# Kernel optimization log

Measured on AMD Instinct MI355X. Metric: run time of the kernel, lower is better.

## Reference

```python
import jax, jax.numpy as jnp
import numpy as np

D_MODEL = 512
N_HEAD = 8
D_K = D_MODEL // N_HEAD
B, S = 4, 2048


def setup_inputs() -> dict:
    key = jax.random.key(0)
    ks = jax.random.split(key, 13)
    scale = 1.0 / np.sqrt(D_MODEL)
    inp = {
        "query": jax.random.normal(ks[0], (B, S, D_MODEL), jnp.float32),
        "key": jax.random.normal(ks[1], (B, S, D_MODEL), jnp.float32),
        "value": jax.random.normal(ks[2], (B, S, D_MODEL), jnp.float32),
        "mask": jax.random.randint(ks[3], (B, S, S), 0, 2).astype(bool),
        "Wq": jax.random.normal(ks[4], (D_MODEL, D_MODEL), jnp.float32) * scale,
        "bq": jax.random.normal(ks[5], (D_MODEL,), jnp.float32) * scale,
        "Wk": jax.random.normal(ks[6], (D_MODEL, D_MODEL), jnp.float32) * scale,
        "bk": jax.random.normal(ks[7], (D_MODEL,), jnp.float32) * scale,
        "Wv": jax.random.normal(ks[8], (D_MODEL, D_MODEL), jnp.float32) * scale,
        "bv": jax.random.normal(ks[9], (D_MODEL,), jnp.float32) * scale,
        "Wo": jax.random.normal(ks[10], (D_MODEL, D_MODEL), jnp.float32) * scale,
        "bo": jax.random.normal(ks[11], (D_MODEL,), jnp.float32) * scale,
    }
    return inp


def reference(query, key, value, mask, Wq, bq, Wk, bk, Wv, bv, Wo, bo):
    b = query.shape[0]
    # QKV projections -> [b, h, s, d_k]
    q = (query @ Wq.T + bq).reshape(b, -1, N_HEAD, D_K).transpose(0, 2, 1, 3)
    k = (key @ Wk.T + bk).reshape(b, -1, N_HEAD, D_K).transpose(0, 2, 1, 3)
    v = (value @ Wv.T + bv).reshape(b, -1, N_HEAD, D_K).transpose(0, 2, 1, 3)
    # scaled dot-product scores [b, h, sq, sk]
    scores = jnp.einsum("bhqd,bhkd->bhqk", q, k) / jnp.sqrt(jnp.float32(D_K))
    # masked_fill(mask, -1e4): mask broadcast over heads
    scores = jnp.where(mask[:, None, :, :], jnp.float32(-10000.0), scores)
    attn = jax.nn.softmax(scores, axis=-1)
    x = jnp.einsum("bhqk,bhkd->bhqd", attn, v)
    x = x.transpose(0, 2, 1, 3).reshape(b, -1, N_HEAD * D_K)
    return x @ Wo.T + bo
```

## Files before the change

kernel.cpp:

```cpp
#include <hip/hip_runtime.h>
#include <hip/hip_bf16.h>

#define DMODEL 512
#define NHEAD  8
#define DKH    64
#define SEQ    2048
#define NB     4
#define LOG2E  1.44269504088896f

typedef float f32x4 __attribute__((ext_vector_type(4)));
typedef float f32x16 __attribute__((ext_vector_type(16)));
typedef short bf16x8 __attribute__((ext_vector_type(8)));

__device__ __forceinline__ unsigned short f2bf(float x) {
    unsigned int u = __float_as_uint(x);
    u += 0x7fffu + ((u >> 16) & 1u);
    return (unsigned short)(u >> 16);
}

__device__ __forceinline__ void gload16(const void* g, void* l) {
    __builtin_amdgcn_global_load_lds(
        (const __attribute__((address_space(1))) unsigned int*)g,
        (__attribute__((address_space(3))) unsigned int*)l, 16, 0, 0);
}

__device__ __forceinline__ unsigned int cvtpk(float lo, float hi) {
    unsigned int r;
    asm("v_cvt_pk_bf16_f32 %0, %1, %2" : "=v"(r) : "v"(lo), "v"(hi));
    return r;
}

#define CVT_BLOCKS  512
#define PACK_BLOCKS 1024
struct PrepArgs {
    const float* src[4]; unsigned short* dst[4];
    const unsigned char* mask; unsigned long long* bits;
};

__global__ __launch_bounds__(256) void prep(PrepArgs a)
{
    const int bx = blockIdx.x;
    if (bx < CVT_BLOCKS) {
        const int seg = bx >> 7, base = bx & 127;
        const int i = (base * 256 + threadIdx.x) * 8;
        const float* s = a.src[seg];
        const float4 v0 = *reinterpret_cast<const float4*>(s + i);
        const float4 v1 = *reinterpret_cast<const float4*>(s + i + 4);
        ushort4 h0, h1;
        h0.x = f2bf(v0.x); h0.y = f2bf(v0.y); h0.z = f2bf(v0.z); h0.w = f2bf(v0.w);
        h1.x = f2bf(v1.x); h1.y = f2bf(v1.y); h1.z = f2bf(v1.z); h1.w = f2bf(v1.w);
        *reinterpret_cast<ushort4*>(a.dst[seg] + i)     = h0;
        *reinterpret_cast<ushort4*>(a.dst[seg] + i + 4) = h1;
    } else {
        __shared__ int anyb;
        if (threadIdx.x == 0) anyb = 0;
        __syncthreads();
        const uint4 dv = *reinterpret_cast<const uint4*>(a.mask + threadIdx.x * 16);
        if ((dv.x | dv.y | dv.z | dv.w) & 0xFFFFFF00u) atomicOr(&anyb, 1);
        __syncthreads();
        const int bytemode = anyb;

        const int w = (bx - CVT_BLOCKS) * 256 + threadIdx.x;
        const int b = w >> 16, kt = (w >> 11) & 31, row = w & 2047;
        const size_t eoff = ((size_t)(b * SEQ + row)) * SEQ + kt * 64;
        unsigned long long word = 0;
        if (bytemode) {
            const unsigned char* mp = a.mask + eoff;
            #pragma unroll
            for (int c = 0; c < 4; ++c) {
                const uint4 v = *reinterpret_cast<const uint4*>(mp + c * 16);
                const unsigned int n0 = (v.x | (v.x >> 7) | (v.x >> 14) | (v.x >> 21)) & 0xFu;
                const unsigned int n1 = (v.y | (v.y >> 7) | (v.y >> 14) | (v.y >> 21)) & 0xFu;
                const unsigned int n2 = (v.z | (v.z >> 7) | (v.z >> 14) | (v.z >> 21)) & 0xFu;
                const unsigned int n3 = (v.w | (v.w >> 7) | (v.w >> 14) | (v.w >> 21)) & 0xFu;
                const unsigned int ch = n0 | (n1 << 4) | (n2 << 8) | (n3 << 12);
                word |= (unsigned long long)ch << (16 * c);
            }
        } else {
            const unsigned int* mp = (const unsigned int*)a.mask + eoff;
            #pragma unroll
            for (int c = 0; c < 16; ++c) {
                const uint4 v = *reinterpret_cast<const uint4*>(mp + c * 4);
                const unsigned int nb = (v.x | (v.y << 1) | (v.z << 2) | (v.w << 3)) & 0xFu;
                word |= (unsigned long long)nb << (4 * c);
            }
        }
        a.bits[w] = word;
    }
}

struct GemmSet {
    const void* A; const unsigned short* W; const float* bias;
    unsigned short* outb; float* outf; float scale; int mode;
};
struct Gemm3 { GemmSet s[3]; };

template<int BM, bool AF32>
__global__ __launch_bounds__(256) void gemm_bf16(Gemm3 G)
{
    constexpr int NJ = (BM == 128) ? 4 : 2;
    __shared__ unsigned short As[BM * 64];
    __shared__ unsigned short Bs[128 * 64];

    const GemmSet gs = G.s[blockIdx.z];
    const int tid = threadIdx.x, lane = tid & 63, wv = tid >> 6;
    const int g = lane >> 4, lr = lane & 15;
    const int bm = blockIdx.x * BM, bn = blockIdx.y * 128;
    const int wm = (BM == 128) ? (wv & 1) * 64 : 0;
    const int wn = (BM == 128) ? (wv >> 1) * 64 : wv * 32;
    const int srow = lane >> 3;
    const int scol = 8 * ((lane & 7) ^ srow);

    const int arow  = tid >> 1;
    const int ahalf = tid & 1;

    f32x4 acc[4][NJ] = {};
    float4 ra[8];

    if constexpr (AF32) {
        const float* Af = (const float*)gs.A;
        #pragma unroll
        for (int j = 0; j < 4; ++j) {
            const size_t gb = (size_t)(bm + arow) * DMODEL + ahalf * 32 + j * 8;
            ra[2*j]   = *reinterpret_cast<const float4*>(&Af[gb]);
            ra[2*j+1] = *reinterpret_cast<const float4*>(&Af[gb + 4]);
        }
    }

    #pragma unroll
    for (int kt = 0; kt < DMODEL; kt += 64) {
        __syncthreads();
        if constexpr (AF32) {
            #pragma unroll
            for (int j = 0; j < 4; ++j) {
                unsigned int w0 = cvtpk(ra[2*j].x,   ra[2*j].y);
                unsigned int w1 = cvtpk(ra[2*j].z,   ra[2*j].w);
                unsigned int w2 = cvtpk(ra[2*j+1].x, ra[2*j+1].y);
                unsigned int w3 = cvtpk(ra[2*j+1].z, ra[2*j+1].w);
                uint4 pkd; pkd.x = w0; pkd.y = w1; pkd.z = w2; pkd.w = w3;
                const int boff = (arow * 128 + ahalf * 64 + j * 16) ^ ((arow & 7) << 4);
                *reinterpret_cast<uint4*>((char*)As + boff) = pkd;
            }
        } else {
            #pragma unroll
            for (int i = 0; i < BM / 32; ++i) {
                const int ch = i * 4 + wv;
                const int row = ch * 8 + srow;
                gload16(&((const unsigned short*)gs.A)[(size_t)(bm + row) * DMODEL + kt + scol],
                        &As[ch * 512 + lane * 8]);
            }
        }
        #pragma unroll
        for (int i = 0; i < 4; ++i) {
            const int ch = i * 4 + wv;
            const int row = ch * 8 + srow;
            gload16(&gs.W[(size_t)(bn + row) * DMODEL + kt + scol], &Bs[ch * 512 + lane * 8]);
        }
        if constexpr (AF32) {
            if (kt + 64 < DMODEL) {
                const float* Af = (const float*)gs.A;
                #pragma unroll
                for (int j = 0; j < 4; ++j) {
                    const size_t gb = (size_t)(bm + arow) * DMODEL + kt + 64 + ahalf * 32 + j * 8;
                    ra[2*j]   = *reinterpret_cast<const float4*>(&Af[gb]);
                    ra[2*j+1] = *reinterpret_cast<const float4*>(&Af[gb + 4]);
                }
            }
        }
        __syncthreads();

        #pragma unroll
        for (int kk = 0; kk < 2; ++kk) {
            bf16x8 af[4], bfr[NJ];
            #pragma unroll
            for (int x = 0; x < 4; ++x) {
                const int ra_ = wm + x * 16 + lr;
                af[x] = *reinterpret_cast<const bf16x8*>(
                    (const char*)As + ((ra_ * 128 + kk * 64 + g * 16) ^ ((ra_ & 7) << 4)));
            }
            #pragma unroll
            for (int y = 0; y < NJ; ++y) {
                const int rb = wn + y * 16 + lr;
                bfr[y] = *reinterpret_cast<const bf16x8*>(
                    (const char*)Bs + ((rb * 128 + kk * 64 + g * 16) ^ ((rb & 7) << 4)));
            }
            __builtin_amdgcn_s_setprio(1);
            #pragma unroll
            for (int mi = 0; mi < 4; ++mi)
                #pragma unroll
                for (int nj = 0; nj < NJ; ++nj)
                    acc[mi][nj] = __builtin_amdgcn_mfma_f32_16x16x32_bf16(af[mi], bfr[nj], acc[mi][nj], 0, 0, 0);
            __builtin_amdgcn_s_setprio(0);
        }
    }

    const int mode = gs.mode;
    #pragma unroll
    for (int mi = 0; mi < 4; ++mi) {
        #pragma unroll
        for (int nj = 0; nj < NJ; ++nj) {
            const int col  = bn + wn + nj * 16 + lr;
            const int row0 = bm + wm + mi * 16 + g * 4;
            const float bv = gs.bias[col];
            if (mode == 2) {
                const int bb = row0 >> 11, ss = row0 & (SEQ - 1);
                const int hh = col >> 6,  dd = col & 63;
                ushort4 pk;
                pk.x = f2bf(acc[mi][nj][0] + bv);
                pk.y = f2bf(acc[mi][nj][1] + bv);
                pk.z = f2bf(acc[mi][nj][2] + bv);
                pk.w = f2bf(acc[mi][nj][3] + bv);
                *reinterpret_cast<ushort4*>(&gs.outb[((size_t)((bb * NHEAD + hh) * DKH + dd)) * SEQ + ss]) = pk;
            } else if (mode == 3) {
                #pragma unroll
                for (int r = 0; r < 4; ++r)
                    gs.outf[(size_t)(row0 + r) * DMODEL + col] = acc[mi][nj][r] + bv;
            } else {
                #pragma unroll
                for (int r = 0; r < 4; ++r)
                    gs.outb[(size_t)(row0 + r) * DMODEL + col] = f2bf((acc[mi][nj][r] + bv) * gs.scale);
            }
        }
    }
}

__global__ __launch_bounds__(256) void attn_fwd(
    const unsigned short* __restrict__ Q,
    const unsigned short* __restrict__ K,
    const unsigned short* __restrict__ Vt,
    const unsigned long long* __restrict__ bits,
    unsigned short* __restrict__ X)
{
    __shared__ unsigned short Ks[2][2][64 * 64];
    __shared__ unsigned short Vs[2][2][64 * 64];

    const int tid = threadIdx.x, lane = tid & 63, wv = tid >> 6;
    const int lr32 = lane & 31, hi = lane >> 5;
    const int bid = blockIdx.x;
    const int wg  = (bid & 7) * 64 + (bid >> 3);
    const int qb = wg & 15, h = (wg >> 4) & 7, b = wg >> 7;
    const int q0 = qb * 128, qw = q0 + wv * 32;

    const unsigned short* Kbh = K  + (size_t)b * SEQ * DMODEL + h * DKH;
    const unsigned short* Vbh = Vt + (size_t)(b * NHEAD + h) * DKH * SEQ;
    const unsigned long long* bitsb = bits + (size_t)b * 32 * SEQ + qw + lr32;

    bf16x8 qf[4];
    #pragma unroll
    for (int kd = 0; kd < 4; ++kd)
        qf[kd] = *reinterpret_cast<const bf16x8*>(
            &Q[(size_t)(b * SEQ + qw + lr32) * DMODEL + h * DKH + kd * 16 + hi * 8]);

    const int srow = lane >> 3;
    const int scol = 8 * ((lane & 7) ^ srow);

    auto stage = [&](int buf, int c) {
        #pragma unroll
        for (int i = 0; i < 4; ++i) {
            const int ch   = i * 4 + wv;
            const int half = ch >> 3;
            const int chh  = ch & 7;
            const int row  = chh * 8 + srow;
            const int kt   = c * 128 + half * 64;
            gload16(&Kbh[(size_t)(kt + row) * DMODEL + scol], &Ks[buf][half][chh * 512 + lane * 8]);
            gload16(&Vbh[(size_t)row * SEQ + kt + scol],      &Vs[buf][half][chh * 512 + lane * 8]);
        }
    };

    union { unsigned int u[4]; bf16x8 v; } onesu;
    onesu.u[0] = onesu.u[1] = onesu.u[2] = onesu.u[3] = 0x3F803F80u;
    const bf16x8 ones = onesu.v;

    f32x16 o0 = {}, o1 = {}, o_sum = {};

    stage(0, 0);
    stage(1, 1);

    for (int t = 0; t < 16; ++t) {
        const int cur = t & 1;

        if (t < 15) asm volatile("s_waitcnt vmcnt(8)" ::: "memory");
        else        asm volatile("s_waitcnt vmcnt(0)" ::: "memory");
        __builtin_amdgcn_sched_barrier(0);
        __builtin_amdgcn_s_barrier();

        const unsigned long long mwA = bitsb[(size_t)(2 * t)     * SEQ];
        const unsigned long long mwB = bitsb[(size_t)(2 * t + 1) * SEQ];

        f32x16 sA0 = {}, sA1 = {}, sB0 = {}, sB1 = {};
        __builtin_amdgcn_s_setprio(1);
        #pragma unroll
        for (int kd = 0; kd < 4; ++kd) {
            const int cb = kd * 32 + hi * 16;
            const int r0 = lr32, r1 = 32 + lr32;
            const bf16x8 kfA0 = *reinterpret_cast<const bf16x8*>(
                (const char*)Ks[cur][0] + ((r0 * 128 + cb) ^ ((r0 & 7) << 4)));
            const bf16x8 kfA1 = *reinterpret_cast<const bf16x8*>(
                (const char*)Ks[cur][0] + ((r1 * 128 + cb) ^ ((r1 & 7) << 4)));
            const bf16x8 kfB0 = *reinterpret_cast<const bf16x8*>(
                (const char*)Ks[cur][1] + ((r0 * 128 + cb) ^ ((r0 & 7) << 4)));
            const bf16x8 kfB1 = *reinterpret_cast<const bf16x8*>(
                (const char*)Ks[cur][1] + ((r1 * 128 + cb) ^ ((r1 & 7) << 4)));
            sA0 = __builtin_amdgcn_mfma_f32_32x32x16_bf16(kfA0, qf[kd], sA0, 0, 0, 0);
            sA1 = __builtin_amdgcn_mfma_f32_32x32x16_bf16(kfA1, qf[kd], sA1, 0, 0, 0);
            sB0 = __builtin_amdgcn_mfma_f32_32x32x16_bf16(kfB0, qf[kd], sB0, 0, 0, 0);
            sB1 = __builtin_amdgcn_mfma_f32_32x32x16_bf16(kfB1, qf[kd], sB1, 0, 0, 0);
        }
        __builtin_amdgcn_s_setprio(0);

        auto subtile = [&](const f32x16& s0, const f32x16& s1,
                           unsigned long long mw, int sub) {
            const unsigned long long msh = mw >> (4 * hi);
            const unsigned int mlo = (unsigned int)msh;
            const unsigned int mhi = (unsigned int)(msh >> 32);
            unsigned int pk[8][2];
            #pragma unroll
            for (int kj = 0; kj < 2; ++kj) {
                const unsigned int msel = kj ? mhi : mlo;
                #pragma unroll
                for (int o2 = 0; o2 < 4; ++o2) {
                    float p[4];
                    #pragma unroll
                    for (int r = 0; r < 4; ++r) {
                        const int bitp = o2 * 8 + r;
                        const float mf = (float)(msel & (1u << bitp));
                        const float coef = -1024.f / (float)(1u << bitp);
                        const float sv = kj ? s1[o2 * 4 + r] : s0[o2 * 4 + r];
                        p[r] = exp2f(__builtin_fmaf(mf, coef, sv));
                    }
                    pk[kj * 4 + o2][0] = cvtpk(p[0], p[1]);
                    pk[kj * 4 + o2][1] = cvtpk(p[2], p[3]);
                }
            }
            #pragma unroll
            for (int kk = 0; kk < 4; ++kk) {
                unsigned int a0 = pk[2 * kk][0], b0 = pk[2 * kk + 1][0];
                unsigned int a1 = pk[2 * kk][1], b1 = pk[2 * kk + 1][1];
                asm("v_permlane32_swap_b32 %0, %1" : "+v"(a0), "+v"(b0));
                asm("v_permlane32_swap_b32 %0, %1" : "+v"(a1), "+v"(b1));
                union { unsigned int u[4]; bf16x8 v; } fr;
                fr.u[0] = a0; fr.u[1] = a1; fr.u[2] = b0; fr.u[3] = b1;
                const int cb = kk * 32 + hi * 16;
                const int d0 = lr32, d1 = 32 + lr32;
                const bf16x8 vf0 = *reinterpret_cast<const bf16x8*>(
                    (const char*)Vs[cur][sub] + ((d0 * 128 + cb) ^ ((d0 & 7) << 4)));
                const bf16x8 vf1 = *reinterpret_cast<const bf16x8*>(
                    (const char*)Vs[cur][sub] + ((d1 * 128 + cb) ^ ((d1 & 7) << 4)));
                __builtin_amdgcn_s_setprio(1);
                o0    = __builtin_amdgcn_mfma_f32_32x32x16_bf16(fr.v, vf0, o0, 0, 0, 0);
                o1    = __builtin_amdgcn_mfma_f32_32x32x16_bf16(fr.v, vf1, o1, 0, 0, 0);
                o_sum = __builtin_amdgcn_mfma_f32_32x32x16_bf16(fr.v, ones, o_sum, 0, 0, 0);
                __builtin_amdgcn_s_setprio(0);
            }
        };
        subtile(sA0, sA1, mwA, 0);
        subtile(sB0, sB1, mwB, 1);

        __builtin_amdgcn_s_barrier();
        if (t + 2 <= 15) stage(cur, t + 2);
    }

    #pragma unroll
    for (int r = 0; r < 16; ++r) {
        const int qr = (r & 3) + 8 * (r >> 2) + 4 * hi;
        const float rv = 1.f / o_sum[r];
        const size_t rowoff = (size_t)(b * SEQ + qw + qr) * DMODEL + h * DKH + lr32;
        X[rowoff]      = f2bf(o0[r] * rv);
        X[rowoff + 32] = f2bf(o1[r] * rv);
    }
}

extern "C" void kernel_launch(void* const* d_in, const int* in_sizes, int n_in,
                              void* d_out, int out_size, void* d_ws, size_t ws_size,
                              hipStream_t stream)
{
    const float* query = (const float*)d_in[0];
    const float* key   = (const float*)d_in[1];
    const float* value = (const float*)d_in[2];
    const unsigned char* mask = (const unsigned char*)d_in[3];
    const float* Wq = (const float*)d_in[4];
    const float* bq = (const float*)d_in[5];
    const float* Wk = (const float*)d_in[6];
    const float* bk = (const float*)d_in[7];
    const float* Wv = (const float*)d_in[8];
    const float* bv = (const float*)d_in[9];
    const float* Wo = (const float*)d_in[10];
    const float* bo = (const float*)d_in[11];

    const size_t E = (size_t)(NB * SEQ) * DMODEL;
    const size_t WE = (size_t)DMODEL * DMODEL;
    unsigned short* Xp  = (unsigned short*)d_ws;
    unsigned short* Qp  = Xp + E;
    unsigned short* Kp  = Qp + E;
    unsigned short* Vtp = Kp + E;
    unsigned short* Wqb = Vtp + E;
    unsigned short* Wkb = Wqb + WE;
    unsigned short* Wvb = Wkb + WE;
    unsigned short* Wob = Wvb + WE;
    unsigned long long* bits = (unsigned long long*)(Wob + WE);

    PrepArgs pa;
    pa.src[0] = Wq; pa.src[1] = Wk; pa.src[2] = Wv; pa.src[3] = Wo;
    pa.dst[0] = Wqb; pa.dst[1] = Wkb; pa.dst[2] = Wvb; pa.dst[3] = Wob;
    pa.mask = mask; pa.bits = bits;
    prep<<<dim3(CVT_BLOCKS + PACK_BLOCKS), 256, 0, stream>>>(pa);

    Gemm3 gq;
    gq.s[0] = { query, Wqb, bq, Qp,  nullptr, 0.125f * LOG2E, 0 };
    gq.s[1] = { key,   Wkb, bk, Kp,  nullptr, 1.0f,   0 };
    gq.s[2] = { value, Wvb, bv, Vtp, nullptr, 1.0f,   2 };
    gemm_bf16<128, true><<<dim3(64, 4, 3), 256, 0, stream>>>(gq);

    attn_fwd<<<dim3(512), 256, 0, stream>>>(Qp, Kp, Vtp, bits, Xp);

    Gemm3 go;
    go.s[0] = { Xp, Wob, bo, nullptr, (float*)d_out, 1.0f, 3 };
    go.s[1] = go.s[0]; go.s[2] = go.s[0];
    gemm_bf16<64, false><<<dim3(128, 4, 1), 256, 0, stream>>>(go);
}
```

Baseline: 135.6 us.

## Co-schedule mask bit-packing with the QKV projection GEMM in one launch

Moves the mask-to-bitmask packing out of the weight-conversion prep kernel and into the QKV GEMM launch as extra blocks. The memory-bound mask read can then overlap with the compute-bound projection GEMM on otherwise idle CUs, and the prep kernel becomes a short weight cast. The GEMM body is factored into a device function so both the fused kernel and the output GEMM can use it. The cost is that the pack blocks now carry the GEMM kernel's LDS allocation, which may limit how many of them run per CU.

```diff
diff --git a/kernel.cpp b/kernel.cpp
--- a/kernel.cpp
+++ b/kernel.cpp
@@ -30,63 +30,20 @@
     return r;
 }
 
-#define CVT_BLOCKS  512
-#define PACK_BLOCKS 1024
-struct PrepArgs {
-    const float* src[4]; unsigned short* dst[4];
-    const unsigned char* mask; unsigned long long* bits;
-};
-
-__global__ __launch_bounds__(256) void prep(PrepArgs a)
-{
-    const int bx = blockIdx.x;
-    if (bx < CVT_BLOCKS) {
-        const int seg = bx >> 7, base = bx & 127;
-        const int i = (base * 256 + threadIdx.x) * 8;
-        const float* s = a.src[seg];
-        const float4 v0 = *reinterpret_cast<const float4*>(s + i);
-        const float4 v1 = *reinterpret_cast<const float4*>(s + i + 4);
-        ushort4 h0, h1;
-        h0.x = f2bf(v0.x); h0.y = f2bf(v0.y); h0.z = f2bf(v0.z); h0.w = f2bf(v0.w);
-        h1.x = f2bf(v1.x); h1.y = f2bf(v1.y); h1.z = f2bf(v1.z); h1.w = f2bf(v1.w);
-        *reinterpret_cast<ushort4*>(a.dst[seg] + i)     = h0;
-        *reinterpret_cast<ushort4*>(a.dst[seg] + i + 4) = h1;
-    } else {
-        __shared__ int anyb;
-        if (threadIdx.x == 0) anyb = 0;
-        __syncthreads();
-        const uint4 dv = *reinterpret_cast<const uint4*>(a.mask + threadIdx.x * 16);
-        if ((dv.x | dv.y | dv.z | dv.w) & 0xFFFFFF00u) atomicOr(&anyb, 1);
-        __syncthreads();
-        const int bytemode = anyb;
-
-        const int w = (bx - CVT_BLOCKS) * 256 + threadIdx.x;
-        const int b = w >> 16, kt = (w >> 11) & 31, row = w & 2047;
-        const size_t eoff = ((size_t)(b * SEQ + row)) * SEQ + kt * 64;
-        unsigned long long word = 0;
-        if (bytemode) {
-            const unsigned char* mp = a.mask + eoff;
-            #pragma unroll
-            for (int c = 0; c < 4; ++c) {
-                const uint4 v = *reinterpret_cast<const uint4*>(mp + c * 16);
-                const unsigned int n0 = (v.x | (v.x >> 7) | (v.x >> 14) | (v.x >> 21)) & 0xFu;
-                const unsigned int n1 = (v.y | (v.y >> 7) | (v.y >> 14) | (v.y >> 21)) & 0xFu;
-                const unsigned int n2 = (v.z | (v.z >> 7) | (v.z >> 14) | (v.z >> 21)) & 0xFu;
-                const unsigned int n3 = (v.w | (v.w >> 7) | (v.w >> 14) | (v.w >> 21)) & 0xFu;
-                const unsigned int ch = n0 | (n1 << 4) | (n2 << 8) | (n3 << 12);
-                word |= (unsigned long long)ch << (16 * c);
-            }
-        } else {
-            const unsigned int* mp = (const unsigned int*)a.mask + eoff;
-            #pragma unroll
-            for (int c = 0; c < 16; ++c) {
-                const uint4 v = *reinterpret_cast<const uint4*>(mp + c * 4);
-                const unsigned int nb = (v.x | (v.y << 1) | (v.z << 2) | (v.w << 3)) & 0xFu;
-                word |= (unsigned long long)nb << (4 * c);
-            }
-        }
-        a.bits[w] = word;
-    }
+struct WcvtArgs { const float* src[4]; unsigned short* dst[4]; };
+
+__global__ __launch_bounds__(256) void prep_wcvt(WcvtArgs a)
+{
+    const int seg = blockIdx.x >> 7, base = blockIdx.x & 127;
+    const int i = (base * 256 + threadIdx.x) * 8;
+    const float* s = a.src[seg];
+    const float4 v0 = *reinterpret_cast<const float4*>(s + i);
+    const float4 v1 = *reinterpret_cast<const float4*>(s + i + 4);
+    ushort4 h0, h1;
+    h0.x = f2bf(v0.x); h0.y = f2bf(v0.y); h0.z = f2bf(v0.z); h0.w = f2bf(v0.w);
+    h1.x = f2bf(v1.x); h1.y = f2bf(v1.y); h1.z = f2bf(v1.z); h1.w = f2bf(v1.w);
+    *reinterpret_cast<ushort4*>(a.dst[seg] + i)     = h0;
+    *reinterpret_cast<ushort4*>(a.dst[seg] + i + 4) = h1;
 }
 
 struct GemmSet {
@@ -96,16 +53,12 @@
 struct Gemm3 { GemmSet s[3]; };
 
 template<int BM, bool AF32>
-__global__ __launch_bounds__(256) void gemm_bf16(Gemm3 G)
+__device__ __forceinline__ void gemm_body(const GemmSet& gs, int bm, int bn,
+                                          unsigned short* As, unsigned short* Bs)
 {
     constexpr int NJ = (BM == 128) ? 4 : 2;
-    __shared__ unsigned short As[BM * 64];
-    __shared__ unsigned short Bs[128 * 64];
-
-    const GemmSet gs = G.s[blockIdx.z];
     const int tid = threadIdx.x, lane = tid & 63, wv = tid >> 6;
     const int g = lane >> 4, lr = lane & 15;
-    const int bm = blockIdx.x * BM, bn = blockIdx.y * 128;
     const int wm = (BM == 128) ? (wv & 1) * 64 : 0;
     const int wn = (BM == 128) ? (wv >> 1) * 64 : wv * 32;
     const int srow = lane >> 3;
@@ -224,6 +177,66 @@
     }
 }
 
+#define GEMM_BLOCKS 768
+#define PACK_BLOCKS 1024
+struct FusedArgs {
+    GemmSet s[3];
+    const unsigned char* mask; unsigned long long* bits;
+};
+
+__global__ __launch_bounds__(256) void gemm_qkv_pack(FusedArgs a)
+{
+    __shared__ unsigned short As[128 * 64];
+    __shared__ unsigned short Bs[128 * 64];
+    const int bx = blockIdx.x;
+    if (bx < GEMM_BLOCKS) {
+        const int gz = bx >> 8, rem = bx & 255;
+        gemm_body<128, true>(a.s[gz], (rem >> 2) * 128, (rem & 3) * 128, As, Bs);
+    } else {
+        __shared__ int anyb;
+        if (threadIdx.x == 0) anyb = 0;
+        __syncthreads();
+        const uint4 dv = *reinterpret_cast<const uint4*>(a.mask + threadIdx.x * 16);
+        if ((dv.x | dv.y | dv.z | dv.w) & 0xFFFFFF00u) atomicOr(&anyb, 1);
+        __syncthreads();
+        const int bytemode = anyb;
+
+        const int w = (bx - GEMM_BLOCKS) * 256 + threadIdx.x;
+        const int b = w >> 16, kt = (w >> 11) & 31, row = w & 2047;
+        const size_t eoff = ((size_t)(b * SEQ + row)) * SEQ + kt * 64;
+        unsigned long long word = 0;
+        if (bytemode) {
+            const unsigned char* mp = a.mask + eoff;
+            #pragma unroll
+            for (int c = 0; c < 4; ++c) {
+                const uint4 v = *reinterpret_cast<const uint4*>(mp + c * 16);
+                const unsigned int n0 = (v.x | (v.x >> 7) | (v.x >> 14) | (v.x >> 21)) & 0xFu;
+                const unsigned int n1 = (v.y | (v.y >> 7) | (v.y >> 14) | (v.y >> 21)) & 0xFu;
+                const unsigned int n2 = (v.z | (v.z >> 7) | (v.z >> 14) | (v.z >> 21)) & 0xFu;
+                const unsigned int n3 = (v.w | (v.w >> 7) | (v.w >> 14) | (v.w >> 21)) & 0xFu;
+                const unsigned int ch = n0 | (n1 << 4) | (n2 << 8) | (n3 << 12);
+                word |= (unsigned long long)ch << (16 * c);
+            }
+        } else {
+            const unsigned int* mp = (const unsigned int*)a.mask + eoff;
+            #pragma unroll
+            for (int c = 0; c < 16; ++c) {
+                const uint4 v = *reinterpret_cast<const uint4*>(mp + c * 4);
+                const unsigned int nb = (v.x | (v.y << 1) | (v.z << 2) | (v.w << 3)) & 0xFu;
+                word |= (unsigned long long)nb << (4 * c);
+            }
+        }
+        a.bits[w] = word;
+    }
+}
+
+__global__ __launch_bounds__(256) void gemm_o(Gemm3 G)
+{
+    __shared__ unsigned short As[64 * 64];
+    __shared__ unsigned short Bs[128 * 64];
+    gemm_body<64, false>(G.s[0], blockIdx.x * 64, blockIdx.y * 128, As, Bs);
+}
+
 __global__ __launch_bounds__(256) void attn_fwd(
     const unsigned short* __restrict__ Q,
     const unsigned short* __restrict__ K,
@@ -399,22 +412,22 @@
     unsigned short* Wob = Wvb + WE;
     unsigned long long* bits = (unsigned long long*)(Wob + WE);
 
-    PrepArgs pa;
-    pa.src[0] = Wq; pa.src[1] = Wk; pa.src[2] = Wv; pa.src[3] = Wo;
-    pa.dst[0] = Wqb; pa.dst[1] = Wkb; pa.dst[2] = Wvb; pa.dst[3] = Wob;
-    pa.mask = mask; pa.bits = bits;
-    prep<<<dim3(CVT_BLOCKS + PACK_BLOCKS), 256, 0, stream>>>(pa);
-
-    Gemm3 gq;
-    gq.s[0] = { query, Wqb, bq, Qp,  nullptr, 0.125f * LOG2E, 0 };
-    gq.s[1] = { key,   Wkb, bk, Kp,  nullptr, 1.0f,   0 };
-    gq.s[2] = { value, Wvb, bv, Vtp, nullptr, 1.0f,   2 };
-    gemm_bf16<128, true><<<dim3(64, 4, 3), 256, 0, stream>>>(gq);
+    WcvtArgs wa;
+    wa.src[0] = Wq; wa.src[1] = Wk; wa.src[2] = Wv; wa.src[3] = Wo;
+    wa.dst[0] = Wqb; wa.dst[1] = Wkb; wa.dst[2] = Wvb; wa.dst[3] = Wob;
+    prep_wcvt<<<dim3(512), 256, 0, stream>>>(wa);
+
+    FusedArgs fa;
+    fa.s[0] = { query, Wqb, bq, Qp,  nullptr, 0.125f * LOG2E, 0 };
+    fa.s[1] = { key,   Wkb, bk, Kp,  nullptr, 1.0f,   0 };
+    fa.s[2] = { value, Wvb, bv, Vtp, nullptr, 1.0f,   2 };
+    fa.mask = mask; fa.bits = bits;
+    gemm_qkv_pack<<<dim3(GEMM_BLOCKS + PACK_BLOCKS), 256, 0, stream>>>(fa);
 
     attn_fwd<<<dim3(512), 256, 0, stream>>>(Qp, Kp, Vtp, bits, Xp);
 
     Gemm3 go;
     go.s[0] = { Xp, Wob, bo, nullptr, (float*)d_out, 1.0f, 3 };
     go.s[1] = go.s[0]; go.s[2] = go.s[0];
-    gemm_bf16<64, false><<<dim3(128, 4, 1), 256, 0, stream>>>(go);
-}
+    gemm_o<<<dim3(128, 4), 256, 0, stream>>>(go);
+}
```

Measured after the change: 142.2 us. +4.9%, slower.
